# Kernel optimization log

Measured on AMD Instinct MI355X. Metric: run time of the kernel, lower is better.

## Reference

```python
import jax, jax.numpy as jnp
import numpy as np

H = 16
D_MODEL = 1024
D_K = D_MODEL // H
B = 4
S = 2048
NEG = -1000000000.0


def setup_inputs() -> dict:
    key = jax.random.key(0)
    ks = jax.random.split(key, 12)
    def lin(k):
        # torch nn.Linear default init: U(-1/sqrt(fan_in), 1/sqrt(fan_in))
        bound = 1.0 / np.sqrt(D_MODEL)
        kw, kb = jax.random.split(k)
        W = jax.random.uniform(kw, (D_MODEL, D_MODEL), jnp.float32, -bound, bound)
        b = jax.random.uniform(kb, (D_MODEL,), jnp.float32, -bound, bound)
        return W, b
    Wq, bq = lin(ks[0]); Wk, bk = lin(ks[1]); Wv, bv = lin(ks[2]); Wo, bo = lin(ks[3])
    return {
        "query": jax.random.normal(ks[4], (B, S, D_MODEL), jnp.float32),
        "key": jax.random.normal(ks[5], (B, S, D_MODEL), jnp.float32),
        "value": jax.random.normal(ks[6], (B, S, D_MODEL), jnp.float32),
        "mask": jax.random.randint(ks[7], (B, S, S), 0, 2, jnp.int32),
        "Wq": Wq, "bq": bq, "Wk": Wk, "bk": bk,
        "Wv": Wv, "bv": bv, "Wo": Wo, "bo": bo,
    }


def reference(query, key, value, mask, Wq, bq, Wk, bk, Wv, bv, Wo, bo):
    # project and split heads: [B,S,D] -> [B,H,S,Dk]
    def proj(x, W, b):
        y = x @ W.T + b
        return y.reshape(B, S, H, D_K).transpose(0, 2, 1, 3)
    q = proj(query, Wq, bq)
    k = proj(key, Wk, bk)
    v = proj(value, Wv, bv)
    m = mask[:, None, :, :]  # [B,1,S,S]
    scores = jnp.einsum("bhqd,bhkd->bhqk", q, k) / jnp.sqrt(jnp.float32(D_K))
    scores = jnp.where(m == 0, NEG, scores)
    p_attn = jax.nn.softmax(scores, axis=-1)
    p_attn = jnp.where(m == 0, 0.0, p_attn)  # faithful to second masked_fill
    x = jnp.einsum("bhqk,bhkd->bhqd", p_attn, v)
    x = x.transpose(0, 2, 1, 3).reshape(B, S, D_MODEL)
    return x @ Wo.T + bo
```

## Files before the change

### kernel.cpp

```cpp
#include <hip/hip_runtime.h>

typedef __attribute__((ext_vector_type(8))) short short8;
typedef __attribute__((ext_vector_type(4))) float f32x4;

#define B_ 4
#define S_ 2048
#define H_ 16
#define DM 1024
#define DK 64

#define QSCALE 0.18033688011112042f

__device__ __forceinline__ unsigned short f2b(float f) {
  unsigned int u = __float_as_uint(f);
  u += 0x7fff + ((u >> 16) & 1);
  return (unsigned short)(u >> 16);
}

__device__ __forceinline__ unsigned int cvtpk_bf16(float lo, float hi) {
  unsigned int r;
  asm("v_cvt_pk_bf16_f32 %0, %1, %2" : "=v"(r) : "v"(lo), "v"(hi));
  return r;
}

__device__ __forceinline__ void gload_lds16(const void* g, void* l) {
  __builtin_amdgcn_global_load_lds(
      (const __attribute__((address_space(1))) unsigned int*)g,
      (__attribute__((address_space(3))) unsigned int*)l, 16, 0, 0);
}

__global__ __launch_bounds__(256) void cvt_kernel(
    const float* __restrict__ a0, const float* __restrict__ a1,
    const float* __restrict__ a2, const float* __restrict__ a3,
    unsigned short* __restrict__ out, int n_per) {
  const float* src = (blockIdx.z == 0) ? a0 : (blockIdx.z == 1) ? a1
                   : (blockIdx.z == 2) ? a2 : a3;
  unsigned short* dst = out + (size_t)blockIdx.z * n_per;
  int i = (blockIdx.x * 256 + threadIdx.x) * 8;
  if (i >= n_per) return;
  float4 x0 = *(const float4*)&src[i];
  float4 x1 = *(const float4*)&src[i + 4];
  alignas(16) unsigned short r[8] = {f2b(x0.x), f2b(x0.y), f2b(x0.z), f2b(x0.w),
                                     f2b(x1.x), f2b(x1.y), f2b(x1.z), f2b(x1.w)};
  *(uint4*)&dst[i] = *(const uint4*)r;
}

__global__ __launch_bounds__(256) void pack_kernel(const int* __restrict__ m,
                                                   unsigned int* __restrict__ out) {
  size_t i = (size_t)blockIdx.x * 256 + threadIdx.x;
  unsigned long long w = __ballot(m[i] != 0);
  if ((threadIdx.x & 31) == 0)
    out[i >> 5] = (unsigned int)(w >> (threadIdx.x & 32));
}

__device__ __forceinline__ void gemm128(
    const unsigned short* __restrict__ A, const unsigned short* __restrict__ W,
    const float* __restrict__ bias, float scale, int mode,
    unsigned short* __restrict__ outb, float* __restrict__ outf) {
  __shared__ unsigned short Sh[128 * 132];
  unsigned short* As = Sh;
  unsigned short* Bs = Sh + 128 * 64;
  const int m0 = blockIdx.x * 128;
  const int n0 = blockIdx.y * 128;
  const int t = threadIdx.x;
  const int lane = t & 63, wave = t >> 6;
  const int lr = lane & 15, quad = lane >> 4;
  const int wm = (wave >> 1) * 64, wn = (wave & 1) * 64;
  const int srow = (lane >> 3);
  const int scol = ((lane & 7) ^ srow) * 8;
  const int cs0 = (quad ^ (lr & 7)) * 8;
  const int cs1 = ((4 + quad) ^ (lr & 7)) * 8;

  const f32x4 zv = {0.f, 0.f, 0.f, 0.f};
  f32x4 acc[4][4];
#pragma unroll
  for (int mt = 0; mt < 4; mt++)
#pragma unroll
    for (int nt = 0; nt < 4; nt++) acc[mt][nt] = zv;

  for (int kb = 0; kb < DM; kb += 64) {
    __syncthreads();
#pragma unroll
    for (int i = 0; i < 4; i++) {
      int c = wave * 4 + i;
      int row = c * 8 + srow;
      gload_lds16(&A[(size_t)(m0 + row) * DM + kb + scol], &As[c * 512]);
      gload_lds16(&W[(size_t)(n0 + row) * DM + kb + scol], &Bs[c * 512]);
    }
    __syncthreads();
#pragma unroll
    for (int ks = 0; ks < 2; ks++) {
      const int cc = ks ? cs1 : cs0;
      short8 af[4], bf[4];
#pragma unroll
      for (int mt = 0; mt < 4; mt++)
        af[mt] = *(const short8*)&As[(wm + mt * 16 + lr) * 64 + cc];
#pragma unroll
      for (int nt = 0; nt < 4; nt++)
        bf[nt] = *(const short8*)&Bs[(wn + nt * 16 + lr) * 64 + cc];
#pragma unroll
      for (int mt = 0; mt < 4; mt++)
#pragma unroll
        for (int nt = 0; nt < 4; nt++)
          acc[mt][nt] = __builtin_amdgcn_mfma_f32_16x16x32_bf16(af[mt], bf[nt], acc[mt][nt], 0, 0, 0);
    }
  }

  if (mode == 1) {
    __syncthreads();
#pragma unroll
    for (int mt = 0; mt < 4; mt++) {
#pragma unroll
      for (int nt = 0; nt < 4; nt++) {
        int n = wn + nt * 16 + lr;
        int m = wm + mt * 16 + quad * 4;
        float bn = bias[n0 + n];
        alignas(8) unsigned short p4[4];
#pragma unroll
        for (int reg = 0; reg < 4; reg++)
          p4[reg] = f2b((acc[mt][nt][reg] + bn) * scale);
        *(uint2*)&Sh[n * 132 + m] = *(const uint2*)p4;
      }
    }
    __syncthreads();
    int n = t >> 1, mh = (t & 1) * 64;
    int gn = n0 + n;
    int h = gn >> 6, dk = gn & 63;
    int b = m0 >> 11, s0 = (m0 & (S_ - 1)) + mh;
    size_t obase = (size_t)((b * H_ + h) * 64 + dk) * S_ + s0;
#pragma unroll
    for (int c = 0; c < 8; c++)
      *(uint4*)&outb[obase + c * 8] = *(const uint4*)&Sh[n * 132 + mh + c * 8];
    return;
  }

#pragma unroll
  for (int mt = 0; mt < 4; mt++) {
#pragma unroll
    for (int nt = 0; nt < 4; nt++) {
#pragma unroll
      for (int reg = 0; reg < 4; reg++) {
        int gm = m0 + wm + mt * 16 + quad * 4 + reg;
        int gn = n0 + wn + nt * 16 + lr;
        float v = (acc[mt][nt][reg] + bias[gn]) * scale;
        if (mode == 0) {
          int b = gm >> 11, s = gm & (S_ - 1);
          int h = gn >> 6, dk = gn & 63;
          outb[(((size_t)(b * H_ + h) * S_ + s) << 6) + dk] = f2b(v);
        } else {
          outf[(size_t)gm * DM + gn] = v;
        }
      }
    }
  }
}

__global__ __launch_bounds__(256) void gemm_qkv_kernel(
    const unsigned short* __restrict__ xb, const unsigned short* __restrict__ wb,
    const float* __restrict__ bq, const float* __restrict__ bk, const float* __restrict__ bv,
    unsigned short* __restrict__ q_out, unsigned short* __restrict__ k_out,
    unsigned short* __restrict__ v_out) {
  int z = blockIdx.z;
  const unsigned short* A = xb + (size_t)z * (B_ * S_ * DM);
  const unsigned short* W = wb + (size_t)z * (DM * DM);
  const float* bias = (z == 0) ? bq : (z == 1) ? bk : bv;
  unsigned short* ob = (z == 0) ? q_out : (z == 1) ? k_out : v_out;
  gemm128(A, W, bias, (z == 0) ? QSCALE : 1.0f, (z == 2) ? 1 : 0, ob, nullptr);
}

__global__ __launch_bounds__(256) void gemm_out_kernel(
    const unsigned short* __restrict__ ab, const unsigned short* __restrict__ wb,
    const float* __restrict__ bo, float* __restrict__ out) {
  gemm128(ab, wb + (size_t)3 * (DM * DM), bo, 1.0f, 2, nullptr, out);
}

__global__ __launch_bounds__(256, 4) void attn_kernel(
    const unsigned short* __restrict__ qb, const unsigned short* __restrict__ kb,
    const unsigned short* __restrict__ vt, const unsigned int* __restrict__ mbits,
    unsigned short* __restrict__ ao) {
  __shared__ unsigned short Ks[2][64 * 64];
  __shared__ unsigned short Vs[2][64 * 64];
  const int bh = blockIdx.x;
  const int b = bh >> 4, h = bh & 15;
  const int t = threadIdx.x, lane = t & 63, wave = t >> 6;
  const int lr = lane & 15, quad = lane >> 4;
  const int q0 = blockIdx.y * 128 + wave * 32;
  const unsigned short* qp = qb + (size_t)bh * S_ * DK;
  const unsigned short* kp = kb + (size_t)bh * S_ * DK;
  const unsigned short* vp = vt + (size_t)bh * DK * S_;
  const unsigned int* mrow = mbits + (size_t)b * S_ * (S_ / 32);

  const int trow = t >> 3;
  const int tsw = ((t & 7) ^ (trow & 7)) * 8;
  const int wbase = wave * 512;
  const int c0 = (quad ^ (lr & 7)) * 8;
  const int c1 = ((4 + quad) ^ (lr & 7)) * 8;
  const int brev = ((quad & 1) << 1) | (quad >> 1);
  const int vc0 = (brev ^ (lr & 7)) * 8;
  const int vc1 = ((4 + brev) ^ (lr & 7)) * 8;
  const int shA = 28 - quad * 4;
  const int shB = 12 - quad * 4;

  short8 qf[2][2];
#pragma unroll
  for (int mt = 0; mt < 2; mt++)
#pragma unroll
    for (int ks = 0; ks < 2; ks++)
      qf[mt][ks] = *(const short8*)&qp[(size_t)(q0 + mt * 16 + lr) * DK + ks * 32 + quad * 8];

  const f32x4 zv = {0.f, 0.f, 0.f, 0.f};
  short8 ones;
#pragma unroll
  for (int i = 0; i < 8; i++) ones[i] = (short)0x3F80;
  f32x4 oacc[2][4], lacc[2];
#pragma unroll
  for (int mt = 0; mt < 2; mt++) {
    lacc[mt] = zv;
#pragma unroll
    for (int nt = 0; nt < 4; nt++) oacc[mt][nt] = zv;
  }

#define STAGE(KT, BUF) do {                                                   \
    int kb2 = (KT) * 64;                                                      \
    gload_lds16(kp + (size_t)(kb2 + trow) * DK + tsw,      &Ks[BUF][wbase]);  \
    gload_lds16(kp + (size_t)(kb2 + 32 + trow) * DK + tsw, &Ks[BUF][2048 + wbase]); \
    gload_lds16(vp + (size_t)trow * S_ + kb2 + tsw,        &Vs[BUF][wbase]);  \
    gload_lds16(vp + (size_t)(32 + trow) * S_ + kb2 + tsw, &Vs[BUF][2048 + wbase]); \
  } while (0)

  auto body = [&](int kt, int buf) {
    uint2 mq[2];
#pragma unroll
    for (int mt = 0; mt < 2; mt++)
      mq[mt] = *(const uint2*)&mrow[(size_t)(q0 + mt * 16 + lr) * (S_ / 32) + kt * 2];

#pragma unroll
    for (int ks = 0; ks < 2; ks++) {
      f32x4 sc[2][2];
#pragma unroll
      for (int ntl = 0; ntl < 2; ntl++) {
        int nt = 2 * ks + ntl;
        short8 kf0 = *(const short8*)&Ks[buf][(nt * 16 + lr) * 64 + c0];
        short8 kf1 = *(const short8*)&Ks[buf][(nt * 16 + lr) * 64 + c1];
#pragma unroll
        for (int mt = 0; mt < 2; mt++) {
          f32x4 z = __builtin_amdgcn_mfma_f32_16x16x32_bf16(kf0, qf[mt][0], zv, 0, 0, 0);
          sc[mt][ntl] = __builtin_amdgcn_mfma_f32_16x16x32_bf16(kf1, qf[mt][1], z, 0, 0, 0);
        }
      }
      short8 pf[2];
#pragma unroll
      for (int mt = 0; mt < 2; mt++) {
        unsigned int w = ks ? mq[mt].y : mq[mt].x;
        unsigned int tA = w << shA;
        unsigned int tB = w << shB;
        float pa[4], pb[4];
#pragma unroll
        for (int r = 0; r < 4; r++) {
          unsigned int sxA = (unsigned int)((int)(tA << (3 - r)) >> 31);
          unsigned int sxB = (unsigned int)((int)(tB << (3 - r)) >> 31);
          pa[r] = __uint_as_float(__float_as_uint(exp2f(sc[mt][0][r])) & sxA);
          pb[r] = __uint_as_float(__float_as_uint(exp2f(sc[mt][1][r])) & sxB);
        }
        unsigned int A0 = cvtpk_bf16(pa[0], pa[1]);
        unsigned int A1 = cvtpk_bf16(pa[2], pa[3]);
        unsigned int B0 = cvtpk_bf16(pb[0], pb[1]);
        unsigned int B1 = cvtpk_bf16(pb[2], pb[3]);
        asm("v_permlane16_swap_b32 %0, %1" : "+v"(A0), "+v"(B0));
        asm("v_permlane16_swap_b32 %0, %1" : "+v"(A1), "+v"(B1));
        union { unsigned int u[4]; short8 s8; } un;
        un.u[0] = A0; un.u[1] = A1; un.u[2] = B0; un.u[3] = B1;
        pf[mt] = un.s8;
      }
#pragma unroll
      for (int mt = 0; mt < 2; mt++)
        lacc[mt] = __builtin_amdgcn_mfma_f32_16x16x32_bf16(pf[mt], ones, lacc[mt], 0, 0, 0);
      const int vc = ks ? vc1 : vc0;
#pragma unroll
      for (int nt = 0; nt < 4; nt++) {
        short8 vf = *(const short8*)&Vs[buf][(nt * 16 + lr) * 64 + vc];
#pragma unroll
        for (int mt = 0; mt < 2; mt++)
          oacc[mt][nt] = __builtin_amdgcn_mfma_f32_16x16x32_bf16(pf[mt], vf, oacc[mt][nt], 0, 0, 0);
      }
    }
  };

  STAGE(0, 0);
  for (int kt = 0; kt < S_ / 64; kt += 2) {
    __syncthreads();
    STAGE(kt + 1, 1);
    body(kt, 0);
    __syncthreads();
    if (kt + 2 < S_ / 64) STAGE(kt + 2, 0);
    body(kt + 1, 1);
  }
#undef STAGE

#pragma unroll
  for (int mt = 0; mt < 2; mt++) {
#pragma unroll
    for (int r = 0; r < 4; r++) {
      float l = lacc[mt][r];
      float inv = (l > 0.f) ? 1.f / l : 0.f;
      int row = q0 + mt * 16 + quad * 4 + r;
#pragma unroll
      for (int nt = 0; nt < 4; nt++)
        ao[((size_t)(b * S_ + row) * DM) + h * 64 + nt * 16 + lr] =
            f2b(oacc[mt][nt][r] * inv);
    }
  }
}

extern "C" void kernel_launch(void* const* d_in, const int* in_sizes, int n_in,
                              void* d_out, int out_size, void* d_ws, size_t ws_size,
                              hipStream_t stream) {
  const float* query = (const float*)d_in[0];
  const float* key   = (const float*)d_in[1];
  const float* value = (const float*)d_in[2];
  const int*   mask  = (const int*)d_in[3];
  const float* Wq = (const float*)d_in[4];
  const float* bq = (const float*)d_in[5];
  const float* Wk = (const float*)d_in[6];
  const float* bk = (const float*)d_in[7];
  const float* Wv = (const float*)d_in[8];
  const float* bv = (const float*)d_in[9];
  const float* Wo = (const float*)d_in[10];
  const float* bo = (const float*)d_in[11];
  float* out = (float*)d_out;
  char* ws = (char*)d_ws;

  unsigned short* qb = (unsigned short*)(ws);
  unsigned short* kbf = (unsigned short*)(ws + 16777216);
  unsigned short* vt = (unsigned short*)(ws + 33554432);
  unsigned short* wb = (unsigned short*)(ws + 50331648);
  unsigned int*   mb = (unsigned int*)(ws + 58720256);
  unsigned short* xb = (unsigned short*)(ws + 60817408);
  unsigned short* ao = (unsigned short*)(ws + 60817408);

  cvt_kernel<<<dim3(4096, 1, 3), 256, 0, stream>>>(query, key, value, nullptr, xb, B_ * S_ * DM);
  cvt_kernel<<<dim3(512, 1, 4), 256, 0, stream>>>(Wq, Wk, Wv, Wo, wb, DM * DM);
  pack_kernel<<<dim3(65536), 256, 0, stream>>>(mask, mb);
  gemm_qkv_kernel<<<dim3(64, 8, 3), 256, 0, stream>>>(xb, wb, bq, bk, bv, qb, kbf, vt);
  attn_kernel<<<dim3(64, 16), 256, 0, stream>>>(qb, kbf, vt, mb, ao);
  gemm_out_kernel<<<dim3(64, 8), 256, 0, stream>>>(ao, wb, bo, out);
}
```

Baseline: 428.2 us.

## Pre-expand mask into per-lane bf16 AND masks in MFMA fragment order

```diff
diff --git a/kernel.cpp b/kernel.cpp
--- a/kernel.cpp
+++ b/kernel.cpp
@@ -21,6 +21,14 @@
   unsigned int r;
   asm("v_cvt_pk_bf16_f32 %0, %1, %2" : "=v"(r) : "v"(lo), "v"(hi));
   return r;
+}
+
+__device__ __forceinline__ float amd_exp2(float x) {
+#if __has_builtin(__builtin_amdgcn_exp2f)
+  return __builtin_amdgcn_exp2f(x);
+#else
+  return exp2f(x);
+#endif
 }
 
 __device__ __forceinline__ void gload_lds16(const void* g, void* l) {
@@ -45,12 +53,27 @@
   *(uint4*)&dst[i] = *(const uint4*)r;
 }
 
-__global__ __launch_bounds__(256) void pack_kernel(const int* __restrict__ m,
-                                                   unsigned int* __restrict__ out) {
-  size_t i = (size_t)blockIdx.x * 256 + threadIdx.x;
-  unsigned long long w = __ballot(m[i] != 0);
-  if ((threadIdx.x & 31) == 0)
-    out[i >> 5] = (unsigned int)(w >> (threadIdx.x & 32));
+__global__ __launch_bounds__(256) void expand_kernel(const int* __restrict__ m,
+                                                     uint4* __restrict__ out) {
+  unsigned int t = blockIdx.x * 256 + threadIdx.x;
+  int lr   = t & 15;
+  int quad = (t >> 4) & 3;
+  int mt   = (t >> 6) & 1;
+  int ks   = (t >> 7) & 1;
+  int kt   = (t >> 8) & 31;
+  int g    = (t >> 13) & 63;
+  int b    = t >> 19;
+  int q = g * 32 + mt * 16 + lr;
+  int kbase = kt * 64 + ks * 32 + quad * 4;
+  const int* row = m + (((size_t)(b * 2048 + q)) << 11) + kbase;
+  int4 m0 = *(const int4*)row;
+  int4 m1 = *(const int4*)(row + 16);
+  uint4 r;
+  r.x = (m0.x ? 0xFFFFu : 0u) | (m0.y ? 0xFFFF0000u : 0u);
+  r.y = (m0.z ? 0xFFFFu : 0u) | (m0.w ? 0xFFFF0000u : 0u);
+  r.z = (m1.x ? 0xFFFFu : 0u) | (m1.y ? 0xFFFF0000u : 0u);
+  r.w = (m1.z ? 0xFFFFu : 0u) | (m1.w ? 0xFFFF0000u : 0u);
+  out[t] = r;
 }
 
 __device__ __forceinline__ void gemm128(
@@ -176,7 +199,7 @@
 
 __global__ __launch_bounds__(256, 4) void attn_kernel(
     const unsigned short* __restrict__ qb, const unsigned short* __restrict__ kb,
-    const unsigned short* __restrict__ vt, const unsigned int* __restrict__ mbits,
+    const unsigned short* __restrict__ vt, const uint4* __restrict__ em,
     unsigned short* __restrict__ ao) {
   __shared__ unsigned short Ks[2][64 * 64];
   __shared__ unsigned short Vs[2][64 * 64];
@@ -188,7 +211,8 @@
   const unsigned short* qp = qb + (size_t)bh * S_ * DK;
   const unsigned short* kp = kb + (size_t)bh * S_ * DK;
   const unsigned short* vp = vt + (size_t)bh * DK * S_;
-  const unsigned int* mrow = mbits + (size_t)b * S_ * (S_ / 32);
+  const int g = blockIdx.y * 4 + wave;
+  const uint4* emrow = em + ((size_t)(b * 64 + g) * 32) * 256 + lane;
 
   const int trow = t >> 3;
   const int tsw = ((t & 7) ^ (trow & 7)) * 8;
@@ -198,8 +222,6 @@
   const int brev = ((quad & 1) << 1) | (quad >> 1);
   const int vc0 = (brev ^ (lr & 7)) * 8;
   const int vc1 = ((4 + brev) ^ (lr & 7)) * 8;
-  const int shA = 28 - quad * 4;
-  const int shB = 12 - quad * 4;
 
   short8 qf[2][2];
 #pragma unroll
@@ -229,10 +251,12 @@
   } while (0)
 
   auto body = [&](int kt, int buf) {
-    uint2 mq[2];
-#pragma unroll
-    for (int mt = 0; mt < 2; mt++)
-      mq[mt] = *(const uint2*)&mrow[(size_t)(q0 + mt * 16 + lr) * (S_ / 32) + kt * 2];
+    uint4 mm[2][2];
+#pragma unroll
+    for (int ks = 0; ks < 2; ks++)
+#pragma unroll
+      for (int mt = 0; mt < 2; mt++)
+        mm[ks][mt] = emrow[(size_t)kt * 256 + (ks * 2 + mt) * 64];
 
 #pragma unroll
     for (int ks = 0; ks < 2; ks++) {
@@ -251,21 +275,18 @@
       short8 pf[2];
 #pragma unroll
       for (int mt = 0; mt < 2; mt++) {
-        unsigned int w = ks ? mq[mt].y : mq[mt].x;
-        unsigned int tA = w << shA;
-        unsigned int tB = w << shB;
         float pa[4], pb[4];
 #pragma unroll
         for (int r = 0; r < 4; r++) {
-          unsigned int sxA = (unsigned int)((int)(tA << (3 - r)) >> 31);
-          unsigned int sxB = (unsigned int)((int)(tB << (3 - r)) >> 31);
-          pa[r] = __uint_as_float(__float_as_uint(exp2f(sc[mt][0][r])) & sxA);
-          pb[r] = __uint_as_float(__float_as_uint(exp2f(sc[mt][1][r])) & sxB);
+          pa[r] = amd_exp2(sc[mt][0][r]);
+          pb[r] = amd_exp2(sc[mt][1][r]);
         }
         unsigned int A0 = cvtpk_bf16(pa[0], pa[1]);
         unsigned int A1 = cvtpk_bf16(pa[2], pa[3]);
         unsigned int B0 = cvtpk_bf16(pb[0], pb[1]);
         unsigned int B1 = cvtpk_bf16(pb[2], pb[3]);
+        const uint4 mv = mm[ks][mt];
+        A0 &= mv.x; A1 &= mv.y; B0 &= mv.z; B1 &= mv.w;
         asm("v_permlane16_swap_b32 %0, %1" : "+v"(A0), "+v"(B0));
         asm("v_permlane16_swap_b32 %0, %1" : "+v"(A1), "+v"(B1));
         union { unsigned int u[4]; short8 s8; } un;
@@ -334,14 +355,14 @@
   unsigned short* kbf = (unsigned short*)(ws + 16777216);
   unsigned short* vt = (unsigned short*)(ws + 33554432);
   unsigned short* wb = (unsigned short*)(ws + 50331648);
-  unsigned int*   mb = (unsigned int*)(ws + 58720256);
-  unsigned short* xb = (unsigned short*)(ws + 60817408);
-  unsigned short* ao = (unsigned short*)(ws + 60817408);
+  unsigned short* xb = (unsigned short*)(ws + 58720256);
+  unsigned short* ao = (unsigned short*)(ws + 58720256);
+  uint4* em = (uint4*)(ws + 75497472);
 
   cvt_kernel<<<dim3(4096, 1, 3), 256, 0, stream>>>(query, key, value, nullptr, xb, B_ * S_ * DM);
   cvt_kernel<<<dim3(512, 1, 4), 256, 0, stream>>>(Wq, Wk, Wv, Wo, wb, DM * DM);
-  pack_kernel<<<dim3(65536), 256, 0, stream>>>(mask, mb);
   gemm_qkv_kernel<<<dim3(64, 8, 3), 256, 0, stream>>>(xb, wb, bq, bk, bv, qb, kbf, vt);
-  attn_kernel<<<dim3(64, 16), 256, 0, stream>>>(qb, kbf, vt, mb, ao);
+  expand_kernel<<<dim3(8192), 256, 0, stream>>>(mask, (uint4*)em);
+  attn_kernel<<<dim3(64, 16), 256, 0, stream>>>(qb, kbf, vt, em, ao);
   gemm_out_kernel<<<dim3(64, 8), 256, 0, stream>>>(ao, wb, bo, out);
 }
```

Result: faster. 381.2 us (-11.0%).
